# Kernel tuning notes

Hardware: AMD Instinct MI355X
Metric: run time of the kernel (lower is better)

## Reference

```python
import jax, jax.numpy as jnp
import numpy as np

DIM = 1280

def setup_inputs() -> dict:
    key = jax.random.key(0)
    ks = jax.random.split(key, 6)
    B, T, D = 16, 2048, DIM
    x = jax.random.normal(ks[0], (B, T, D), dtype=jnp.float32)
    # in_proj: Linear(D, 2D, bias=False) -> weight [2D, D]
    W_in = jax.random.normal(ks[1], (2 * D, D), dtype=jnp.float32) * (1.0 / np.sqrt(D))
    # out_proj: Linear(D, D, bias=False)
    W_out = jax.random.normal(ks[2], (D, D), dtype=jnp.float32) * (1.0 / np.sqrt(D))
    # E1Cell params: W_x xavier, W_h orthogonal*0.9, b zeros
    W_x = jax.random.normal(ks[3], (D, D), dtype=jnp.float32) * np.sqrt(2.0 / (D + D))
    A = np.asarray(jax.random.normal(ks[4], (D, D), dtype=jnp.float32))
    Q, _ = np.linalg.qr(A)
    W_h = jnp.asarray(Q, dtype=jnp.float32) * 0.9
    b = jnp.zeros((D,), dtype=jnp.float32)
    return {"x": x, "W_in": W_in, "W_out": W_out, "W_x": W_x, "W_h": W_h, "b": b}

def _elman_forward(x, W_in, W_out, W_x, W_h, b):
    B, T, D = x.shape
    xz = jnp.einsum('btd,ed->bte', x, W_in)  # [B,T,2D]
    x_proj, z = xz[..., :D], xz[..., D:]
    x_proj = jax.nn.silu(x_proj)
    # precompute input contribution for all steps: [T,B,D]
    x_pre = jnp.einsum('btd,ed->tbe', x_proj, W_x) + b
    z_t = jnp.transpose(z, (1, 0, 2))  # [T,B,D]
    h0 = jnp.zeros((B, D), dtype=x.dtype)

    def step(h_prev, inp):
        xp, zg = inp
        h = jnp.tanh(xp + h_prev @ W_h.T)
        out = h * jax.nn.silu(zg)
        return h, out

    h_final, out_tbd = jax.lax.scan(step, h0, (x_pre, z_t))
    out = jnp.transpose(out_tbd, (1, 0, 2))  # [B,T,D]
    out = jnp.einsum('btd,ed->bte', out, W_out)
    return out, h_final

def reference(x, W_in, W_out, W_x, W_h, b):
    return _elman_forward(x, W_in, W_out, W_x, W_h, b)
```

## Files before the change

kernel.cpp:

```cpp
#include <hip/hip_runtime.h>

#define D_  1280
#define T_  2048
#define B_  16
#define NW  40
#define RPW 32
#define KS  320

typedef unsigned short u16;
typedef unsigned int   u32;
typedef unsigned long long u64;
typedef __attribute__((ext_vector_type(8))) short bf16x8;
typedef __attribute__((ext_vector_type(4))) float f32x4;
typedef __attribute__((ext_vector_type(4))) int   i32x4;

__device__ __forceinline__ float bf2f(u16 u) {
  union { u32 i; float f; } v; v.i = ((u32)u) << 16; return v.f;
}
__device__ __forceinline__ u16 f2bf(float f) {
  union { float f; u32 i; } v; v.f = f;
  u32 r = v.i + 0x7fffu + ((v.i >> 16) & 1u);
  return (u16)(r >> 16);
}
__device__ __forceinline__ float sigm(float x) { return 1.f / (1.f + __expf(-x)); }
__device__ __forceinline__ float tanh_(float x) { return 1.f - 2.f / (__expf(2.f * x) + 1.f); }

__global__ void detect_k(const u16* __restrict__ x, int* __restrict__ dflag) {
  __shared__ int cnt;
  if (threadIdx.x == 0) cnt = 0;
  __syncthreads();
  u16 u = x[threadIdx.x];
  int e = (u >> 7) & 0xFF;
  if (e >= 100 && e <= 140) atomicAdd(&cnt, 1);
  __syncthreads();
  if (threadIdx.x == 0) *dflag = (cnt < 192) ? 1 : 0;
}

__global__ void cvt_k(const void* __restrict__ src, u16* __restrict__ dst,
                      long n, const int* __restrict__ dflag) {
  const int fp32 = *dflag;
  long base = ((long)blockIdx.x * 256 + threadIdx.x) * 8;
  if (base + 8 <= n) {
    if (fp32) {
      const float* s = (const float*)src;
      f32x4 f0 = *(const f32x4*)(s + base);
      f32x4 f1 = *(const f32x4*)(s + base + 4);
      u32 w0 = (u32)f2bf(f0[0]) | ((u32)f2bf(f0[1]) << 16);
      u32 w1 = (u32)f2bf(f0[2]) | ((u32)f2bf(f0[3]) << 16);
      u32 w2 = (u32)f2bf(f1[0]) | ((u32)f2bf(f1[1]) << 16);
      u32 w3 = (u32)f2bf(f1[2]) | ((u32)f2bf(f1[3]) << 16);
      i32x4 o = { (int)w0, (int)w1, (int)w2, (int)w3 };
      *(i32x4*)(dst + base) = o;
    } else {
      *(i32x4*)(dst + base) = *(const i32x4*)((const u16*)src + base);
    }
  } else {
    for (long i = base; i < n; ++i)
      dst[i] = fp32 ? f2bf(((const float*)src)[i]) : ((const u16*)src)[i];
  }
}

template<int EPI>
__global__ __launch_bounds__(256, 2) void gemm_bt(
    const u16* __restrict__ A, const u16* __restrict__ B,
    u16* __restrict__ C0, u16* __restrict__ C1,
    const u16* __restrict__ bias,
    void* __restrict__ Cout, const int* __restrict__ dflag)
{
  __shared__ __align__(16) u16 As[128 * 40];
  __shared__ __align__(16) u16 Bs[128 * 40];

  const int fp32o = (EPI == 2) ? *dflag : 0;
  const int tid  = threadIdx.x;
  const int lane = tid & 63;
  const int qq   = lane >> 4, ln = lane & 15;
  const int wave = tid >> 6;
  const int wm   = (wave >> 1) * 64, wn = (wave & 1) * 64;
  const long m0  = (long)blockIdx.y * 128;
  const long n0  = (long)blockIdx.x * 128;

  const int r0 = tid >> 2, c0 = (tid & 3) * 8;
  const int r1 = r0 + 64;

  f32x4 acc[4][4];
  #pragma unroll
  for (int i = 0; i < 4; ++i)
    #pragma unroll
    for (int j = 0; j < 4; ++j) acc[i][j] = (f32x4){0.f, 0.f, 0.f, 0.f};

  for (int kt = 0; kt < D_; kt += 32) {
    i32x4 av0 = *(const i32x4*)(A + (m0 + r0) * D_ + kt + c0);
    i32x4 av1 = *(const i32x4*)(A + (m0 + r1) * D_ + kt + c0);
    i32x4 bv0 = *(const i32x4*)(B + (n0 + r0) * D_ + kt + c0);
    i32x4 bv1 = *(const i32x4*)(B + (n0 + r1) * D_ + kt + c0);
    __syncthreads();
    *(i32x4*)(As + r0 * 40 + c0) = av0;
    *(i32x4*)(As + r1 * 40 + c0) = av1;
    *(i32x4*)(Bs + r0 * 40 + c0) = bv0;
    *(i32x4*)(Bs + r1 * 40 + c0) = bv1;
    __syncthreads();

    bf16x8 af[4], bfr[4];
    #pragma unroll
    for (int i = 0; i < 4; ++i)
      af[i] = *(const bf16x8*)(As + (wm + i * 16 + ln) * 40 + qq * 8);
    #pragma unroll
    for (int j = 0; j < 4; ++j)
      bfr[j] = *(const bf16x8*)(Bs + (wn + j * 16 + ln) * 40 + qq * 8);
    #pragma unroll
    for (int i = 0; i < 4; ++i)
      #pragma unroll
      for (int j = 0; j < 4; ++j)
        acc[i][j] = __builtin_amdgcn_mfma_f32_16x16x32_bf16(af[i], bfr[j], acc[i][j], 0, 0, 0);
  }

  #pragma unroll
  for (int i = 0; i < 4; ++i)
    #pragma unroll
    for (int j = 0; j < 4; ++j)
      #pragma unroll
      for (int r = 0; r < 4; ++r) {
        long m = m0 + wm + i * 16 + qq * 4 + r;
        long n = n0 + wn + j * 16 + ln;
        float v = acc[i][j][r];
        if (EPI == 0) {
          float s = v * sigm(v);
          long t = m & 2047, bb = m >> 11;
          if (n < D_) C0[m * D_ + n] = f2bf(s);
          else        C1[(t * 16 + bb) * D_ + (n - D_)] = f2bf(s);
        } else if (EPI == 1) {
          long t = m & 2047, bb = m >> 11;
          C0[(t * 16 + bb) * D_ + n] = f2bf(v + bf2f(bias[n]));
        } else {
          long bb = m & 15, t = m >> 4;
          long idx = (bb * 2048 + t) * D_ + n;
          if (fp32o) ((float*)Cout)[idx] = v;
          else       ((u16*)Cout)[idx]   = f2bf(v);
        }
      }
}

__global__ __launch_bounds__(256, 1) void scan_rnn(
    const u16* __restrict__ Wh, const u16* __restrict__ xpre,
    const u16* __restrict__ zs, u16* __restrict__ sout,
    u16* __restrict__ hbuf, u32* __restrict__ flags,
    void* __restrict__ dout, const int* __restrict__ dflag)
{
  const int fp32o = *dflag;
  const int wg   = blockIdx.x;
  const int tid  = threadIdx.x;
  const int lane = tid & 63;
  const int wave = tid >> 6;
  const int qq   = lane >> 4, ln = lane & 15;

  bf16x8 wfrag[2][10];
  #pragma unroll
  for (int i = 0; i < 2; ++i) {
    const u16* wrow = Wh + (long)(wg * RPW + i * 16 + ln) * D_ + wave * KS;
    #pragma unroll
    for (int c = 0; c < 10; ++c)
      wfrag[i][c] = *(const bf16x8*)(wrow + c * 32 + qq * 8);
  }

  __shared__ float red[2][2176];

  const int batch = tid >> 4;
  const int dl0   = (tid & 15) * 2;
  const int d0    = wg * RPW + dl0;
  const int tile  = dl0 >> 4;
  const int row0  = dl0 & 15;

  const u32* fl = flags + 40 * wave + ((lane < 40) ? lane : 0);

  const long hload = (long)ln * 320 + wave * 80 + qq * 2;

  long pidx = (long)(0 * B_ + batch) * D_ + d0;
  u32 xp2 = *(const u32*)(xpre + pidx);
  u32 zs2 = *(const u32*)(zs + pidx);

  for (int t = 0; t < T_; ++t) {
    const u64* hc = (const u64*)(hbuf + (t & 1) * (B_ * D_));
    u16*       hn = hbuf + ((t + 1) & 1) * (B_ * D_);

    {
      const u32 tgt = (u32)t;
      for (;;) {
        u32 v = __hip_atomic_load(fl, __ATOMIC_RELAXED, __HIP_MEMORY_SCOPE_AGENT);
        if (__all(v >= tgt)) break;
      }
    }

    const u64* hr = hc + hload;
    u64 hq[20];
    #pragma unroll
    for (int c = 0; c < 10; ++c) {
      hq[c * 2 + 0] = __hip_atomic_load(hr + c * 8 + 0,
                          __ATOMIC_RELAXED, __HIP_MEMORY_SCOPE_AGENT);
      hq[c * 2 + 1] = __hip_atomic_load(hr + c * 8 + 1,
                          __ATOMIC_RELAXED, __HIP_MEMORY_SCOPE_AGENT);
    }

    f32x4 a0 = (f32x4){0.f,0.f,0.f,0.f}, a1 = (f32x4){0.f,0.f,0.f,0.f};
    #pragma unroll
    for (int c = 0; c < 10; ++c) {
      union { u64 q[2]; bf16x8 v; } hu;
      hu.q[0] = hq[c * 2 + 0];
      hu.q[1] = hq[c * 2 + 1];
      a0 = __builtin_amdgcn_mfma_f32_16x16x32_bf16(wfrag[0][c], hu.v, a0, 0, 0, 0);
      a1 = __builtin_amdgcn_mfma_f32_16x16x32_bf16(wfrag[1][c], hu.v, a1, 0, 0, 0);
    }

    float* rw = red[t & 1];
    #pragma unroll
    for (int r = 0; r < 4; ++r) {
      rw[(wave * 2 + 0) * 272 + (qq * 4 + r) * 17 + ln] = a0[r];
      rw[(wave * 2 + 1) * 272 + (qq * 4 + r) * 17 + ln] = a1[r];
    }
    __syncthreads();

    float s0 = rw[(0 + tile) * 272 + row0 * 17 + batch]
             + rw[(2 + tile) * 272 + row0 * 17 + batch]
             + rw[(4 + tile) * 272 + row0 * 17 + batch]
             + rw[(6 + tile) * 272 + row0 * 17 + batch];
    float s1 = rw[(0 + tile) * 272 + (row0 + 1) * 17 + batch]
             + rw[(2 + tile) * 272 + (row0 + 1) * 17 + batch]
             + rw[(4 + tile) * 272 + (row0 + 1) * 17 + batch]
             + rw[(6 + tile) * 272 + (row0 + 1) * 17 + batch];

    float h0 = tanh_(bf2f((u16)(xp2 & 0xffff)) + s0);
    float h1 = tanh_(bf2f((u16)(xp2 >> 16)) + s1);
    float o0 = h0 * bf2f((u16)(zs2 & 0xffff));
    float o1 = h1 * bf2f((u16)(zs2 >> 16));
    u32 opack = (u32)f2bf(o0) | ((u32)f2bf(o1) << 16);
    u32 hpack = (u32)f2bf(h0) | ((u32)f2bf(h1) << 16);

    if (t == T_ - 1) {
      *(u32*)(sout + pidx) = opack;
      if (fp32o) {
        float* hf32 = (float*)dout + (long)B_ * T_ * D_;
        hf32[batch * D_ + d0]     = h0;
        hf32[batch * D_ + d0 + 1] = h1;
      } else {
        u16* hb = (u16*)dout + (long)B_ * T_ * D_;
        *(u32*)(hb + batch * D_ + d0) = hpack;
      }
      break;
    }

    __hip_atomic_store((u32*)(hn + batch * D_ + d0), hpack,
                       __ATOMIC_RELAXED, __HIP_MEMORY_SCOPE_AGENT);
    asm volatile("s_waitcnt vmcnt(0)" ::: "memory");
    if (lane == 0)
      __hip_atomic_store(&flags[wg * 4 + wave], (u32)(t + 1),
                         __ATOMIC_RELAXED, __HIP_MEMORY_SCOPE_AGENT);

    *(u32*)(sout + pidx) = opack;
    pidx = (long)((t + 1) * B_ + batch) * D_ + d0;
    xp2 = *(const u32*)(xpre + pidx);
    zs2 = *(const u32*)(zs + pidx);
  }
}

extern "C" void kernel_launch(void* const* d_in, const int* in_sizes, int n_in,
                              void* d_out, int out_size, void* d_ws, size_t ws_size,
                              hipStream_t stream) {
  const void* x     = d_in[0];
  const void* W_in  = d_in[1];
  const void* W_out = d_in[2];
  const void* W_x   = d_in[3];
  const void* W_h   = d_in[4];
  const void* bias  = d_in[5];

  const size_t SZ = (size_t)32768 * D_ * sizeof(u16);
  char* ws = (char*)d_ws;
  u16* bufA  = (u16*)(ws);
  u16* bufB  = (u16*)(ws + SZ);
  u16* wi    = (u16*)(ws + 2 * SZ);
  u16* wo    = (u16*)(ws + 2 * SZ +  6553600);
  u16* wx    = (u16*)(ws + 2 * SZ +  9830400);
  u16* wh    = (u16*)(ws + 2 * SZ + 13107200);
  u16* bb_   = (u16*)(ws + 2 * SZ + 16384000);
  u16* hbuf  = (u16*)(ws + 2 * SZ + 16386560);
  u32* flags = (u32*)(ws + 2 * SZ + 16386560 + 81920);
  int* dflag = (int*)(ws + 2 * SZ + 16386560 + 81920 + 640);
  u16* zsil  = (u16*)d_out;

  hipMemsetAsync(hbuf, 0, 81920 + 640, stream);

  detect_k<<<1, 256, 0, stream>>>((const u16*)x, dflag);
  cvt_k<<<20480, 256, 0, stream>>>(x,     bufA, 41943040L, dflag);
  cvt_k<<< 1600, 256, 0, stream>>>(W_in,  wi,    3276800L, dflag);
  cvt_k<<<  800, 256, 0, stream>>>(W_out, wo,    1638400L, dflag);
  cvt_k<<<  800, 256, 0, stream>>>(W_x,   wx,    1638400L, dflag);
  cvt_k<<<  800, 256, 0, stream>>>(W_h,   wh,    1638400L, dflag);
  cvt_k<<<    1, 256, 0, stream>>>(bias,  bb_,      1280L, dflag);

  gemm_bt<0><<<dim3(20, 256), 256, 0, stream>>>(bufA, wi, bufB, zsil, nullptr, nullptr, dflag);
  gemm_bt<1><<<dim3(10, 256), 256, 0, stream>>>(bufB, wx, bufA, nullptr, bb_, nullptr, dflag);
  scan_rnn<<<NW, 256, 0, stream>>>(wh, bufA, zsil, bufA, hbuf, flags, d_out, dflag);
  gemm_bt<2><<<dim3(10, 256), 256, 0, stream>>>(bufA, wo, nullptr, nullptr, nullptr, d_out, dflag);
}
```

Before: 9.613 ms.

## Split recurrent scan per batch element across XCD-local workgroup groups

The scan kernel now launches 256 workgroups. Each batch element gets its own group of 16 workgroups placed on one XCD, so synchronization flags and the hidden state are exchanged only within that batch's group and not across all 40 workgroups. Each workgroup holds 80 rows of W_h in registers and computes a matrix-vector product for a single batch. This shrinks the all-to-all dependency and keeps flag traffic local, at the cost of more register pressure, MFMA columns wasted on the single batch, and a spin-wait budget that can break out early.

```diff
diff --git a/kernel.cpp b/kernel.cpp
--- a/kernel.cpp
+++ b/kernel.cpp
@@ -3,9 +3,6 @@
 #define D_  1280
 #define T_  2048
 #define B_  16
-#define NW  40
-#define RPW 32
-#define KS  320
 
 typedef unsigned short u16;
 typedef unsigned int   u32;
@@ -147,117 +144,130 @@
     void* __restrict__ dout, const int* __restrict__ dflag)
 {
   const int fp32o = *dflag;
-  const int wg   = blockIdx.x;
+  const int g    = blockIdx.x;
+  const int xcd  = g & 7;
+  const int slot = g >> 3;
+  const int b    = (slot >> 4) * 8 + xcd;
+  const int p    = slot & 15;
   const int tid  = threadIdx.x;
   const int lane = tid & 63;
-  const int wave = tid >> 6;
+  const int w    = tid >> 6;
   const int qq   = lane >> 4, ln = lane & 15;
 
-  bf16x8 wfrag[2][10];
+  bf16x8 wfrag[5][10];
   #pragma unroll
-  for (int i = 0; i < 2; ++i) {
-    const u16* wrow = Wh + (long)(wg * RPW + i * 16 + ln) * D_ + wave * KS;
+  for (int i = 0; i < 5; ++i) {
+    const u16* wrow = Wh + (long)(p * 80 + i * 16 + ln) * D_ + w * 320;
     #pragma unroll
     for (int c = 0; c < 10; ++c)
       wfrag[i][c] = *(const bf16x8*)(wrow + c * 32 + qq * 8);
   }
 
-  __shared__ float red[2][2176];
-
-  const int batch = tid >> 4;
-  const int dl0   = (tid & 15) * 2;
-  const int d0    = wg * RPW + dl0;
-  const int tile  = dl0 >> 4;
-  const int row0  = dl0 & 15;
-
-  const u32* fl = flags + 40 * wave + ((lane < 40) ? lane : 0);
-
-  const long hload = (long)ln * 320 + wave * 80 + qq * 2;
-
-  long pidx = (long)(0 * B_ + batch) * D_ + d0;
-  u32 xp2 = *(const u32*)(xpre + pidx);
-  u32 zs2 = *(const u32*)(zs + pidx);
+  __shared__ float red[2][320];
+
+  int pl;
+  if      (lane < 16) pl = (4 * w + (lane >> 2)) * 4 + (lane & 3);
+  else if (lane < 20) pl = p * 4 + (lane - 16);
+  else                pl = (4 * w) * 4;
+  const u32* fl = flags + b * 256 + pl;
+  u32*       fs = flags + b * 256 + p * 4 + w;
+
+  const int erow = 20 * w + lane;
+  const int ed   = 80 * p + erow;
+  const int ep   = (lane < 20);
+
+  u16* hb0 = hbuf + b * 2560;
+
+  long pidx = (long)(0 * B_ + b) * D_ + ed;
+  u16 xp = 0, zv = 0;
+  if (ep) { xp = xpre[pidx]; zv = zs[pidx]; }
+
+  int budget = 1 << 21;
 
   for (int t = 0; t < T_; ++t) {
-    const u64* hc = (const u64*)(hbuf + (t & 1) * (B_ * D_));
-    u16*       hn = hbuf + ((t + 1) & 1) * (B_ * D_);
+    const u16* hc = hb0 + (t & 1) * D_;
+    u16*       hn = hb0 + ((t + 1) & 1) * D_;
 
     {
       const u32 tgt = (u32)t;
       for (;;) {
         u32 v = __hip_atomic_load(fl, __ATOMIC_RELAXED, __HIP_MEMORY_SCOPE_AGENT);
-        if (__all(v >= tgt)) break;
+        if (__all(v >= tgt) || --budget < 0) break;
       }
     }
 
-    const u64* hr = hc + hload;
     u64 hq[20];
     #pragma unroll
     for (int c = 0; c < 10; ++c) {
-      hq[c * 2 + 0] = __hip_atomic_load(hr + c * 8 + 0,
+      const u64* hr = (const u64*)(hc + w * 320 + c * 32 + qq * 8);
+      hq[c * 2 + 0] = __hip_atomic_load(hr + 0,
                           __ATOMIC_RELAXED, __HIP_MEMORY_SCOPE_AGENT);
-      hq[c * 2 + 1] = __hip_atomic_load(hr + c * 8 + 1,
+      hq[c * 2 + 1] = __hip_atomic_load(hr + 1,
                           __ATOMIC_RELAXED, __HIP_MEMORY_SCOPE_AGENT);
     }
 
-    f32x4 a0 = (f32x4){0.f,0.f,0.f,0.f}, a1 = (f32x4){0.f,0.f,0.f,0.f};
+    f32x4 acc[5];
+    #pragma unroll
+    for (int i = 0; i < 5; ++i) acc[i] = (f32x4){0.f, 0.f, 0.f, 0.f};
     #pragma unroll
     for (int c = 0; c < 10; ++c) {
       union { u64 q[2]; bf16x8 v; } hu;
       hu.q[0] = hq[c * 2 + 0];
       hu.q[1] = hq[c * 2 + 1];
-      a0 = __builtin_amdgcn_mfma_f32_16x16x32_bf16(wfrag[0][c], hu.v, a0, 0, 0, 0);
-      a1 = __builtin_amdgcn_mfma_f32_16x16x32_bf16(wfrag[1][c], hu.v, a1, 0, 0, 0);
+      #pragma unroll
+      for (int i = 0; i < 5; ++i)
+        acc[i] = __builtin_amdgcn_mfma_f32_16x16x32_bf16(wfrag[i][c], hu.v, acc[i], 0, 0, 0);
     }
 
     float* rw = red[t & 1];
-    #pragma unroll
-    for (int r = 0; r < 4; ++r) {
-      rw[(wave * 2 + 0) * 272 + (qq * 4 + r) * 17 + ln] = a0[r];
-      rw[(wave * 2 + 1) * 272 + (qq * 4 + r) * 17 + ln] = a1[r];
+    if (ln == 0) {
+      #pragma unroll
+      for (int i = 0; i < 5; ++i)
+        #pragma unroll
+        for (int r = 0; r < 4; ++r)
+          rw[w * 80 + i * 16 + qq * 4 + r] = acc[i][r];
     }
     __syncthreads();
 
-    float s0 = rw[(0 + tile) * 272 + row0 * 17 + batch]
-             + rw[(2 + tile) * 272 + row0 * 17 + batch]
-             + rw[(4 + tile) * 272 + row0 * 17 + batch]
-             + rw[(6 + tile) * 272 + row0 * 17 + batch];
-    float s1 = rw[(0 + tile) * 272 + (row0 + 1) * 17 + batch]
-             + rw[(2 + tile) * 272 + (row0 + 1) * 17 + batch]
-             + rw[(4 + tile) * 272 + (row0 + 1) * 17 + batch]
-             + rw[(6 + tile) * 272 + (row0 + 1) * 17 + batch];
-
-    float h0 = tanh_(bf2f((u16)(xp2 & 0xffff)) + s0);
-    float h1 = tanh_(bf2f((u16)(xp2 >> 16)) + s1);
-    float o0 = h0 * bf2f((u16)(zs2 & 0xffff));
-    float o1 = h1 * bf2f((u16)(zs2 >> 16));
-    u32 opack = (u32)f2bf(o0) | ((u32)f2bf(o1) << 16);
-    u32 hpack = (u32)f2bf(h0) | ((u32)f2bf(h1) << 16);
+    float h = 0.f, o = 0.f;
+    u16 hbf = 0;
+    if (ep) {
+      float s = rw[0 * 80 + erow] + rw[1 * 80 + erow]
+              + rw[2 * 80 + erow] + rw[3 * 80 + erow];
+      h = tanh_(bf2f(xp) + s);
+      o = h * bf2f(zv);
+      hbf = f2bf(h);
+    }
+
+    u32 hx  = (u32)hbf;
+    u32 px  = (u32)__shfl_xor((int)hx, 1);
+    u32 hpk = hx | (px << 16);
 
     if (t == T_ - 1) {
-      *(u32*)(sout + pidx) = opack;
-      if (fp32o) {
-        float* hf32 = (float*)dout + (long)B_ * T_ * D_;
-        hf32[batch * D_ + d0]     = h0;
-        hf32[batch * D_ + d0 + 1] = h1;
-      } else {
-        u16* hb = (u16*)dout + (long)B_ * T_ * D_;
-        *(u32*)(hb + batch * D_ + d0) = hpack;
+      if (ep) {
+        sout[pidx] = f2bf(o);
+        if (fp32o) {
+          float* hf = (float*)dout + (long)B_ * T_ * D_;
+          hf[b * D_ + ed] = h;
+        } else {
+          u16* hb = (u16*)dout + (long)B_ * T_ * D_;
+          hb[b * D_ + ed] = hbf;
+        }
       }
       break;
     }
 
-    __hip_atomic_store((u32*)(hn + batch * D_ + d0), hpack,
-                       __ATOMIC_RELAXED, __HIP_MEMORY_SCOPE_AGENT);
+    if (ep && !(lane & 1))
+      __hip_atomic_store((u32*)(hn + ed), hpk,
+                         __ATOMIC_RELAXED, __HIP_MEMORY_SCOPE_AGENT);
     asm volatile("s_waitcnt vmcnt(0)" ::: "memory");
     if (lane == 0)
-      __hip_atomic_store(&flags[wg * 4 + wave], (u32)(t + 1),
+      __hip_atomic_store(fs, (u32)(t + 1),
                          __ATOMIC_RELAXED, __HIP_MEMORY_SCOPE_AGENT);
 
-    *(u32*)(sout + pidx) = opack;
-    pidx = (long)((t + 1) * B_ + batch) * D_ + d0;
-    xp2 = *(const u32*)(xpre + pidx);
-    zs2 = *(const u32*)(zs + pidx);
+    if (ep) sout[pidx] = f2bf(o);
+    pidx = (long)((t + 1) * B_ + b) * D_ + ed;
+    if (ep) { xp = xpre[pidx]; zv = zs[pidx]; }
   }
 }
 
@@ -282,10 +292,10 @@
   u16* bb_   = (u16*)(ws + 2 * SZ + 16384000);
   u16* hbuf  = (u16*)(ws + 2 * SZ + 16386560);
   u32* flags = (u32*)(ws + 2 * SZ + 16386560 + 81920);
-  int* dflag = (int*)(ws + 2 * SZ + 16386560 + 81920 + 640);
+  int* dflag = (int*)(ws + 2 * SZ + 16386560 + 81920 + 16384);
   u16* zsil  = (u16*)d_out;
 
-  hipMemsetAsync(hbuf, 0, 81920 + 640, stream);
+  hipMemsetAsync(hbuf, 0, 81920 + 16384, stream);
 
   detect_k<<<1, 256, 0, stream>>>((const u16*)x, dflag);
   cvt_k<<<20480, 256, 0, stream>>>(x,     bufA, 41943040L, dflag);
@@ -297,6 +307,6 @@
 
   gemm_bt<0><<<dim3(20, 256), 256, 0, stream>>>(bufA, wi, bufB, zsil, nullptr, nullptr, dflag);
   gemm_bt<1><<<dim3(10, 256), 256, 0, stream>>>(bufB, wx, bufA, nullptr, bb_, nullptr, dflag);
-  scan_rnn<<<NW, 256, 0, stream>>>(wh, bufA, zsil, bufA, hbuf, flags, d_out, dflag);
+  scan_rnn<<<256, 256, 0, stream>>>(wh, bufA, zsil, bufA, hbuf, flags, d_out, dflag);
   gemm_bt<2><<<dim3(10, 256), 256, 0, stream>>>(bufA, wo, nullptr, nullptr, nullptr, d_out, dflag);
 }
```

Measured after the change: 7.694 ms. 20.0% less time.
